# Kernel optimization log

Measured on AMD Instinct MI355X. Metric: run time of the kernel, lower is better.

## Reference

```python
import jax, jax.numpy as jnp
import numpy as np

WH, WW = 7, 7
L = WH * WW            # 49 tokens per window
C = 128                # embedding dim
H = 32                 # heads
HD = C // H            # head dim = 4
BN = 4096              # batch * num_windows


def _relative_position_index(wh, ww):
    coords = np.stack(np.meshgrid(np.arange(wh), np.arange(ww), indexing='ij'))  # [2,wh,ww]
    flat = coords.reshape(2, -1)                     # [2, L]
    rel = flat[:, :, None] - flat[:, None, :]        # [2, L, L]
    rel = rel.transpose(1, 2, 0).copy()              # [L, L, 2]
    rel[:, :, 0] += wh - 1
    rel[:, :, 1] += ww - 1
    rel[:, :, 0] *= 2 * ww - 1
    return jnp.asarray(rel.sum(-1), dtype=jnp.int32)  # [L, L]


REL_IDX = _relative_position_index(WH, WW)


def setup_inputs() -> dict:
    key = jax.random.key(0)
    k1, k2, k3, k4 = jax.random.split(key, 4)
    x = jax.random.normal(k1, (BN, L, C), dtype=jnp.float32)
    W_qkv = jax.random.normal(k2, (C, 3 * C), dtype=jnp.float32) * (C ** -0.5)
    b_qkv = jnp.zeros((3 * C,), dtype=jnp.float32)
    W_proj = jax.random.normal(k3, (C, C), dtype=jnp.float32) * (C ** -0.5)
    b_proj = jnp.zeros((C,), dtype=jnp.float32)
    bias_table = jax.random.normal(k4, ((2 * WH - 1) * (2 * WW - 1), H), dtype=jnp.float32) * 0.02
    return {"x": x, "W_qkv": W_qkv, "b_qkv": b_qkv, "W_proj": W_proj,
            "b_proj": b_proj, "bias_table": bias_table}


def reference(x, W_qkv, b_qkv, W_proj, b_proj, bias_table):
    bn, l, c = x.shape
    scale = HD ** -0.5
    qkv = x @ W_qkv + b_qkv                                   # [BN, L, 3C]
    qkv = qkv.reshape(bn, l, 3, H, HD).transpose(2, 0, 3, 1, 4)  # [3, BN, H, L, HD]
    q, k, v = qkv[0], qkv[1], qkv[2]
    attn = jnp.einsum('bhqd,bhkd->bhqk', q * scale, k)        # [BN, H, L, L]
    rel_bias = bias_table[REL_IDX]                            # [L, L, H]
    attn = attn + rel_bias.transpose(2, 0, 1)[None]           # add [1, H, L, L]
    attn = jax.nn.softmax(attn, axis=-1)
    out = jnp.einsum('bhqk,bhkd->bhqd', attn, v)              # [BN, H, L, HD]
    out = out.transpose(0, 2, 1, 3).reshape(bn, l, c)         # [BN, L, C]
    return out @ W_proj + b_proj
```

## Files before the change

kernel.cpp:

```cpp
#include <hip/hip_runtime.h>
#include <hip/hip_bf16.h>
#include <stdint.h>

#define L 49
#define C 128
#define H 32

typedef __attribute__((ext_vector_type(8))) short bf16x8;
typedef __attribute__((ext_vector_type(4))) float f32x4;

#define XP 136
#define VTP 72
#define QKP 264

#define LOG2E 1.44269504f

__device__ __forceinline__ uint32_t rbits(float f) {
  return __builtin_bit_cast(uint32_t, f) + 0x8000u;
}
__device__ __forceinline__ uint32_t pack2(float a, float b) {
  return __builtin_amdgcn_perm(rbits(b), rbits(a), 0x07060302u);
}
__device__ __forceinline__ ushort bf1(float a) { return (ushort)(rbits(a) >> 16); }

__device__ __forceinline__ bf16x8 mk_frag(uint2 d, bool valid) {
  union { uint32_t u[4]; bf16x8 v; } r;
  r.u[0] = valid ? d.x : 0u;
  r.u[1] = valid ? d.y : 0u;
  r.u[2] = 0u; r.u[3] = 0u;
  return r.v;
}
__device__ __forceinline__ bf16x8 zero8() {
  union { uint32_t u[4]; bf16x8 v; } r;
  r.u[0] = r.u[1] = r.u[2] = r.u[3] = 0u;
  return r.v;
}
__device__ __forceinline__ bf16x8 ones8() {
  union { uint32_t u[4]; bf16x8 v; } r;
  r.u[0] = r.u[1] = r.u[2] = r.u[3] = 0x3F803F80u;
  return r.v;
}

__global__ void __launch_bounds__(256) prep_weights_kernel(
    const float* __restrict__ Wqkv, const float* __restrict__ Wproj,
    ushort* __restrict__ ws) {
  int i = blockIdx.x * 256 + threadIdx.x;
  if (i < 384 * 128) {
    int n = i >> 7, k = i & 127;
    ws[i] = bf1(Wqkv[k * 384 + n]);
  } else {
    int j = i - 384 * 128;
    if (j < 128 * 128) {
      int n = j >> 7, k = j & 127;
      ws[49152 + j] = bf1(Wproj[k * 128 + n]);
    }
  }
}

__global__ void __launch_bounds__(256) prep_bias_kernel(
    const float* __restrict__ bt, float* __restrict__ biasx) {
  int i = blockIdx.x * 256 + threadIdx.x;
  int r = i & 3, lane = (i >> 2) & 63, t = i >> 8;
  int nt = t & 3, mt = (t >> 2) & 3, h = t >> 4;
  int q = nt * 16 + (lane & 15);
  int k = mt * 16 + ((lane >> 4) & 3) * 4 + r;
  float v = -1e30f;
  if (q < L && k < L) {
    int qi = q / 7, qj = q % 7, ki = k / 7, kj = k % 7;
    int idx = (qi - ki + 6) * 13 + (qj - kj + 6);
    v = bt[idx * H + h] * LOG2E;
  }
  biasx[i] = v;
}

__device__ __forceinline__ void head_body(
    f32x4 (&acc)[4][4], int h, const ushort* qk, const ushort* vt,
    char* pw, ushort* qk_mut, int lr, int lg) {
  bf16x8 ka[4], qb[4];
  #pragma unroll
  for (int mt = 0; mt < 4; ++mt) {
    int row = mt * 16 + lr; if (row > 48) row = 48;
    uint2 d = *(const uint2*)&qk[row * QKP + 128 + h * 4];
    ka[mt] = mk_frag(d, lg == 0);
  }
  #pragma unroll
  for (int nt = 0; nt < 4; ++nt) {
    int row = nt * 16 + lr; if (row > 48) row = 48;
    uint2 d = *(const uint2*)&qk[row * QKP + h * 4];
    qb[nt] = mk_frag(d, lg == 0);
  }
  __builtin_amdgcn_s_setprio(1);
  #pragma unroll
  for (int nt = 0; nt < 4; ++nt)
    #pragma unroll
    for (int mt = 0; mt < 4; ++mt)
      acc[mt][nt] = __builtin_amdgcn_mfma_f32_16x16x32_bf16(ka[mt], qb[nt], acc[mt][nt], 0, 0, 0);
  __builtin_amdgcn_s_setprio(0);
  bf16x8 va[2];
  #pragma unroll
  for (int ks = 0; ks < 2; ++ks) {
    bf16x8 t = *(const bf16x8*)&vt[(h * 4 + (lr & 3)) * VTP + ks * 32 + lg * 8];
    va[ks] = (lr < 4) ? t : ((lr == 4) ? ones8() : zero8());
  }
  #pragma unroll
  for (int nt = 0; nt < 4; ++nt) {
    #pragma unroll
    for (int mt = 0; mt < 4; ++mt) {
      uint32_t d0, d1;
      if (mt < 3) {
        uint32_t u0 = rbits(__builtin_amdgcn_exp2f(acc[mt][nt][0]));
        uint32_t u1 = rbits(__builtin_amdgcn_exp2f(acc[mt][nt][1]));
        uint32_t u2 = rbits(__builtin_amdgcn_exp2f(acc[mt][nt][2]));
        uint32_t u3 = rbits(__builtin_amdgcn_exp2f(acc[mt][nt][3]));
        d0 = __builtin_amdgcn_perm(u1, u0, 0x07060302u);
        d1 = __builtin_amdgcn_perm(u3, u2, 0x07060302u);
      } else {
        float e0 = __builtin_amdgcn_exp2f(acc[mt][nt][0]);
        d0 = pack2(e0, 0.0f);
        d1 = 0u;
      }
      int byte = lr * 128 + mt * 32 + lg * 8;
      byte ^= (lr & 7) << 4;
      *(uint2*)(pw + byte) = make_uint2(d0, d1);
    }
    f32x4 oo = {0.f, 0.f, 0.f, 0.f};
    __builtin_amdgcn_s_setprio(1);
    #pragma unroll
    for (int ks = 0; ks < 2; ++ks) {
      int byte = lr * 128 + ks * 64 + lg * 16;
      byte ^= (lr & 7) << 4;
      bf16x8 pb = *(const bf16x8*)(pw + byte);
      oo = __builtin_amdgcn_mfma_f32_16x16x32_bf16(va[ks], pb, oo, 0, 0, 0);
    }
    __builtin_amdgcn_s_setprio(0);
    float den = __shfl_xor(oo[0], 16);
    if (lg == 0) {
      float iv = __builtin_amdgcn_rcpf(den);
      int q = nt * 16 + lr;
      if (q < L) {
        uint2 od = make_uint2(pack2(oo[0] * iv, oo[1] * iv),
                              pack2(oo[2] * iv, oo[3] * iv));
        *(uint2*)&qk_mut[q * QKP + h * 4] = od;
      }
    }
  }
}

__global__ void __launch_bounds__(256, 3) win_attn_kernel(
    const float* __restrict__ x,
    const float* __restrict__ b_qkv,
    const float* __restrict__ b_proj,
    const ushort* __restrict__ wqkvT,
    const ushort* __restrict__ wprojT,
    const float* __restrict__ biasx,
    float* __restrict__ out) {
  __shared__ alignas(16) ushort s_xv[C * VTP];
  __shared__ alignas(16) ushort qk[L * QKP];
  __shared__ alignas(16) ushort p_lds[4][16 * 64];

  ushort* xa = s_xv;
  ushort* vt = s_xv;

  const int tid = threadIdx.x;
  const int w = blockIdx.x;
  const int wv = tid >> 6;
  const int l = tid & 63;
  const int lr = l & 15;
  const int lg = l >> 4;

  {
    const float4* xv = (const float4*)(x + (size_t)w * (L * C));
    for (int i = tid; i < L * C / 4; i += 256) {
      float4 v = xv[i];
      int e = i * 4;
      int r = e >> 7, c = e & 127;
      uint2 u = make_uint2(pack2(v.x, v.y), pack2(v.z, v.w));
      *(uint2*)&xa[r * XP + c] = u;
    }
  }
  __syncthreads();

  {
    bf16x8 af[4][4];
    #pragma unroll
    for (int mt = 0; mt < 4; ++mt) {
      int row = mt * 16 + lr; if (row > 48) row = 48;
      #pragma unroll
      for (int kk = 0; kk < 4; ++kk)
        af[mt][kk] = *(const bf16x8*)&xa[row * XP + kk * 32 + lg * 8];
    }
    __syncthreads();
    #pragma unroll 2
    for (int ntl = 0; ntl < 6; ++ntl) {
      int nt = (ntl < 2) ? (wv * 2 + ntl)
             : (ntl < 4) ? (8 + wv * 2 + (ntl - 2))
                         : (16 + wv * 2 + (ntl - 4));
      int ncol = nt * 16 + lr;
      const ushort* bp = wqkvT + ncol * C + lg * 8;
      bf16x8 b0 = *(const bf16x8*)(bp);
      bf16x8 b1 = *(const bf16x8*)(bp + 32);
      bf16x8 b2 = *(const bf16x8*)(bp + 64);
      bf16x8 b3 = *(const bf16x8*)(bp + 96);
      float bias = b_qkv[ncol];
      float sc = (ncol < 128) ? 0.5f * LOG2E : 1.0f;
      #pragma unroll
      for (int mt = 0; mt < 4; ++mt) {
        f32x4 acc = {0.f, 0.f, 0.f, 0.f};
        acc = __builtin_amdgcn_mfma_f32_16x16x32_bf16(af[mt][0], b0, acc, 0, 0, 0);
        acc = __builtin_amdgcn_mfma_f32_16x16x32_bf16(af[mt][1], b1, acc, 0, 0, 0);
        acc = __builtin_amdgcn_mfma_f32_16x16x32_bf16(af[mt][2], b2, acc, 0, 0, 0);
        acc = __builtin_amdgcn_mfma_f32_16x16x32_bf16(af[mt][3], b3, acc, 0, 0, 0);
        if (ncol < 256) {
          #pragma unroll
          for (int r = 0; r < 4; ++r) {
            int row = mt * 16 + lg * 4 + r;
            if (row < L) qk[row * QKP + ncol] = bf1((acc[r] + bias) * sc);
          }
        } else {
          int kbase = mt * 16 + lg * 4;
          uint2 pv = make_uint2(pack2(acc[0] + bias, acc[1] + bias),
                                pack2(acc[2] + bias, acc[3] + bias));
          *(uint2*)&vt[(ncol - 256) * VTP + kbase] = pv;
        }
      }
    }
  }

  {
    char* pw = (char*)&p_lds[wv][0];
    const f32x4* bx = (const f32x4*)biasx;
    #pragma unroll 2
    for (int hh = 0; hh < 8; ++hh) {
      int h = wv * 8 + hh;
      f32x4 acc[4][4];
      #pragma unroll
      for (int mt = 0; mt < 4; ++mt)
        #pragma unroll
        for (int nt = 0; nt < 4; ++nt)
          acc[mt][nt] = bx[(h * 16 + mt * 4 + nt) * 64 + l];
      head_body(acc, h, qk, vt, pw, qk, lr, lg);
    }
  }
  __syncthreads();

  {
    bf16x8 pf[4][4];
    #pragma unroll
    for (int mt = 0; mt < 4; ++mt) {
      int row = mt * 16 + lr; if (row > 48) row = 48;
      #pragma unroll
      for (int kk = 0; kk < 4; ++kk)
        pf[mt][kk] = *(const bf16x8*)&qk[row * QKP + kk * 32 + lg * 8];
    }
    float* outw = out + (size_t)w * (L * C);
    #pragma unroll 2
    for (int ntl = 0; ntl < 2; ++ntl) {
      int ncol = (wv * 2 + ntl) * 16 + lr;
      const ushort* bp = wprojT + ncol * C + lg * 8;
      bf16x8 b0 = *(const bf16x8*)(bp);
      bf16x8 b1 = *(const bf16x8*)(bp + 32);
      bf16x8 b2 = *(const bf16x8*)(bp + 64);
      bf16x8 b3 = *(const bf16x8*)(bp + 96);
      float bias = b_proj[ncol];
      #pragma unroll
      for (int mt = 0; mt < 4; ++mt) {
        f32x4 acc = {0.f, 0.f, 0.f, 0.f};
        acc = __builtin_amdgcn_mfma_f32_16x16x32_bf16(pf[mt][0], b0, acc, 0, 0, 0);
        acc = __builtin_amdgcn_mfma_f32_16x16x32_bf16(pf[mt][1], b1, acc, 0, 0, 0);
        acc = __builtin_amdgcn_mfma_f32_16x16x32_bf16(pf[mt][2], b2, acc, 0, 0, 0);
        acc = __builtin_amdgcn_mfma_f32_16x16x32_bf16(pf[mt][3], b3, acc, 0, 0, 0);
        #pragma unroll
        for (int r = 0; r < 4; ++r) {
          int row = mt * 16 + lg * 4 + r;
          if (row < L) outw[row * C + ncol] = acc[r] + bias;
        }
      }
    }
  }
}

extern "C" void kernel_launch(void* const* d_in, const int* in_sizes, int n_in,
                              void* d_out, int out_size, void* d_ws, size_t ws_size,
                              hipStream_t stream) {
  const float* x     = (const float*)d_in[0];
  const float* Wqkv  = (const float*)d_in[1];
  const float* bqkv  = (const float*)d_in[2];
  const float* Wproj = (const float*)d_in[3];
  const float* bproj = (const float*)d_in[4];
  const float* btab  = (const float*)d_in[5];
  float* out = (float*)d_out;
  ushort* ws = (ushort*)d_ws;
  float* biasx = (float*)(ws + 65536);

  int bn = in_sizes[0] / (L * C);

  hipLaunchKernelGGL(prep_weights_kernel, dim3(256), dim3(256), 0, stream,
                     Wqkv, Wproj, ws);
  hipLaunchKernelGGL(prep_bias_kernel, dim3(512), dim3(256), 0, stream,
                     btab, biasx);
  hipLaunchKernelGGL(win_attn_kernel, dim3(bn), dim3(256), 0, stream,
                     x, bqkv, bproj, ws, ws + 49152, biasx, out);
}
```

Measured before the change: 170.0 us.

## Make window attention kernel persistent with register prefetch of next window

Turns the one-block-per-window launch into a persistent grid of up to 768 blocks, each looping over windows with stride npers. Within each iteration, the next window's x tile is loaded into registers while the current window's QKV, attention and projection run. This overlaps global loads with compute and removes per-block launch and prologue costs. In exchange it holds 7 float4 values live in registers across the whole loop, which adds register pressure under the 3-blocks-per-CU launch bound and could cause spills or lower occupancy.

```diff
diff --git a/kernel.cpp b/kernel.cpp
--- a/kernel.cpp
+++ b/kernel.cpp
@@ -5,6 +5,7 @@
 #define L 49
 #define C 128
 #define H 32
+#define NPERS 768
 
 typedef __attribute__((ext_vector_type(8))) short bf16x8;
 typedef __attribute__((ext_vector_type(4))) float f32x4;
@@ -153,7 +154,8 @@
     const ushort* __restrict__ wqkvT,
     const ushort* __restrict__ wprojT,
     const float* __restrict__ biasx,
-    float* __restrict__ out) {
+    float* __restrict__ out,
+    int bn, int npers) {
   __shared__ alignas(16) ushort s_xv[C * VTP];
   __shared__ alignas(16) ushort qk[L * QKP];
   __shared__ alignas(16) ushort p_lds[4][16 * 64];
@@ -162,120 +164,142 @@
   ushort* vt = s_xv;
 
   const int tid = threadIdx.x;
-  const int w = blockIdx.x;
   const int wv = tid >> 6;
   const int l = tid & 63;
   const int lr = l & 15;
   const int lg = l >> 4;
 
+  float4 xr[7];
+  int w = blockIdx.x;
   {
     const float4* xv = (const float4*)(x + (size_t)w * (L * C));
-    for (int i = tid; i < L * C / 4; i += 256) {
-      float4 v = xv[i];
-      int e = i * 4;
-      int r = e >> 7, c = e & 127;
-      uint2 u = make_uint2(pack2(v.x, v.y), pack2(v.z, v.w));
-      *(uint2*)&xa[r * XP + c] = u;
-    }
-  }
-  __syncthreads();
-
-  {
-    bf16x8 af[4][4];
-    #pragma unroll
-    for (int mt = 0; mt < 4; ++mt) {
-      int row = mt * 16 + lr; if (row > 48) row = 48;
+    #pragma unroll
+    for (int j = 0; j < 7; ++j) {
+      int i = tid + j * 256;
+      if (i < L * C / 4) xr[j] = xv[i];
+    }
+  }
+
+  for (; w < bn; ) {
+    #pragma unroll
+    for (int j = 0; j < 7; ++j) {
+      int i = tid + j * 256;
+      if (i < L * C / 4) {
+        float4 v = xr[j];
+        int e = i * 4;
+        int r = e >> 7, c = e & 127;
+        *(uint2*)&xa[r * XP + c] = make_uint2(pack2(v.x, v.y), pack2(v.z, v.w));
+      }
+    }
+    const int wn = w + npers;
+    if (wn < bn) {
+      const float4* xv = (const float4*)(x + (size_t)wn * (L * C));
       #pragma unroll
-      for (int kk = 0; kk < 4; ++kk)
-        af[mt][kk] = *(const bf16x8*)&xa[row * XP + kk * 32 + lg * 8];
+      for (int j = 0; j < 7; ++j) {
+        int i = tid + j * 256;
+        if (i < L * C / 4) xr[j] = xv[i];
+      }
     }
     __syncthreads();
-    #pragma unroll 2
-    for (int ntl = 0; ntl < 6; ++ntl) {
-      int nt = (ntl < 2) ? (wv * 2 + ntl)
-             : (ntl < 4) ? (8 + wv * 2 + (ntl - 2))
-                         : (16 + wv * 2 + (ntl - 4));
-      int ncol = nt * 16 + lr;
-      const ushort* bp = wqkvT + ncol * C + lg * 8;
-      bf16x8 b0 = *(const bf16x8*)(bp);
-      bf16x8 b1 = *(const bf16x8*)(bp + 32);
-      bf16x8 b2 = *(const bf16x8*)(bp + 64);
-      bf16x8 b3 = *(const bf16x8*)(bp + 96);
-      float bias = b_qkv[ncol];
-      float sc = (ncol < 128) ? 0.5f * LOG2E : 1.0f;
+
+    {
+      bf16x8 af[4][4];
       #pragma unroll
       for (int mt = 0; mt < 4; ++mt) {
-        f32x4 acc = {0.f, 0.f, 0.f, 0.f};
-        acc = __builtin_amdgcn_mfma_f32_16x16x32_bf16(af[mt][0], b0, acc, 0, 0, 0);
-        acc = __builtin_amdgcn_mfma_f32_16x16x32_bf16(af[mt][1], b1, acc, 0, 0, 0);
-        acc = __builtin_amdgcn_mfma_f32_16x16x32_bf16(af[mt][2], b2, acc, 0, 0, 0);
-        acc = __builtin_amdgcn_mfma_f32_16x16x32_bf16(af[mt][3], b3, acc, 0, 0, 0);
-        if (ncol < 256) {
+        int row = mt * 16 + lr; if (row > 48) row = 48;
+        #pragma unroll
+        for (int kk = 0; kk < 4; ++kk)
+          af[mt][kk] = *(const bf16x8*)&xa[row * XP + kk * 32 + lg * 8];
+      }
+      __syncthreads();
+      #pragma unroll 2
+      for (int ntl = 0; ntl < 6; ++ntl) {
+        int nt = (ntl < 2) ? (wv * 2 + ntl)
+               : (ntl < 4) ? (8 + wv * 2 + (ntl - 2))
+                           : (16 + wv * 2 + (ntl - 4));
+        int ncol = nt * 16 + lr;
+        const ushort* bp = wqkvT + ncol * C + lg * 8;
+        bf16x8 b0 = *(const bf16x8*)(bp);
+        bf16x8 b1 = *(const bf16x8*)(bp + 32);
+        bf16x8 b2 = *(const bf16x8*)(bp + 64);
+        bf16x8 b3 = *(const bf16x8*)(bp + 96);
+        float bias = b_qkv[ncol];
+        float sc = (ncol < 128) ? 0.5f * LOG2E : 1.0f;
+        #pragma unroll
+        for (int mt = 0; mt < 4; ++mt) {
+          f32x4 acc = {0.f, 0.f, 0.f, 0.f};
+          acc = __builtin_amdgcn_mfma_f32_16x16x32_bf16(af[mt][0], b0, acc, 0, 0, 0);
+          acc = __builtin_amdgcn_mfma_f32_16x16x32_bf16(af[mt][1], b1, acc, 0, 0, 0);
+          acc = __builtin_amdgcn_mfma_f32_16x16x32_bf16(af[mt][2], b2, acc, 0, 0, 0);
+          acc = __builtin_amdgcn_mfma_f32_16x16x32_bf16(af[mt][3], b3, acc, 0, 0, 0);
+          if (ncol < 256) {
+            #pragma unroll
+            for (int r = 0; r < 4; ++r) {
+              int row = mt * 16 + lg * 4 + r;
+              if (row < L) qk[row * QKP + ncol] = bf1((acc[r] + bias) * sc);
+            }
+          } else {
+            int kbase = mt * 16 + lg * 4;
+            uint2 pv = make_uint2(pack2(acc[0] + bias, acc[1] + bias),
+                                  pack2(acc[2] + bias, acc[3] + bias));
+            *(uint2*)&vt[(ncol - 256) * VTP + kbase] = pv;
+          }
+        }
+      }
+    }
+
+    {
+      char* pw = (char*)&p_lds[wv][0];
+      const f32x4* bx = (const f32x4*)biasx;
+      #pragma unroll 2
+      for (int hh = 0; hh < 8; ++hh) {
+        int h = wv * 8 + hh;
+        f32x4 acc[4][4];
+        #pragma unroll
+        for (int mt = 0; mt < 4; ++mt)
+          #pragma unroll
+          for (int nt = 0; nt < 4; ++nt)
+            acc[mt][nt] = bx[(h * 16 + mt * 4 + nt) * 64 + l];
+        head_body(acc, h, qk, vt, pw, qk, lr, lg);
+      }
+    }
+    __syncthreads();
+
+    {
+      bf16x8 pf[4][4];
+      #pragma unroll
+      for (int mt = 0; mt < 4; ++mt) {
+        int row = mt * 16 + lr; if (row > 48) row = 48;
+        #pragma unroll
+        for (int kk = 0; kk < 4; ++kk)
+          pf[mt][kk] = *(const bf16x8*)&qk[row * QKP + kk * 32 + lg * 8];
+      }
+      float* outw = out + (size_t)w * (L * C);
+      #pragma unroll 2
+      for (int ntl = 0; ntl < 2; ++ntl) {
+        int ncol = (wv * 2 + ntl) * 16 + lr;
+        const ushort* bp = wprojT + ncol * C + lg * 8;
+        bf16x8 b0 = *(const bf16x8*)(bp);
+        bf16x8 b1 = *(const bf16x8*)(bp + 32);
+        bf16x8 b2 = *(const bf16x8*)(bp + 64);
+        bf16x8 b3 = *(const bf16x8*)(bp + 96);
+        float bias = b_proj[ncol];
+        #pragma unroll
+        for (int mt = 0; mt < 4; ++mt) {
+          f32x4 acc = {0.f, 0.f, 0.f, 0.f};
+          acc = __builtin_amdgcn_mfma_f32_16x16x32_bf16(pf[mt][0], b0, acc, 0, 0, 0);
+          acc = __builtin_amdgcn_mfma_f32_16x16x32_bf16(pf[mt][1], b1, acc, 0, 0, 0);
+          acc = __builtin_amdgcn_mfma_f32_16x16x32_bf16(pf[mt][2], b2, acc, 0, 0, 0);
+          acc = __builtin_amdgcn_mfma_f32_16x16x32_bf16(pf[mt][3], b3, acc, 0, 0, 0);
           #pragma unroll
           for (int r = 0; r < 4; ++r) {
             int row = mt * 16 + lg * 4 + r;
-            if (row < L) qk[row * QKP + ncol] = bf1((acc[r] + bias) * sc);
+            if (row < L) outw[row * C + ncol] = acc[r] + bias;
           }
-        } else {
-          int kbase = mt * 16 + lg * 4;
-          uint2 pv = make_uint2(pack2(acc[0] + bias, acc[1] + bias),
-                                pack2(acc[2] + bias, acc[3] + bias));
-          *(uint2*)&vt[(ncol - 256) * VTP + kbase] = pv;
         }
       }
     }
-  }
-
-  {
-    char* pw = (char*)&p_lds[wv][0];
-    const f32x4* bx = (const f32x4*)biasx;
-    #pragma unroll 2
-    for (int hh = 0; hh < 8; ++hh) {
-      int h = wv * 8 + hh;
-      f32x4 acc[4][4];
-      #pragma unroll
-      for (int mt = 0; mt < 4; ++mt)
-        #pragma unroll
-        for (int nt = 0; nt < 4; ++nt)
-          acc[mt][nt] = bx[(h * 16 + mt * 4 + nt) * 64 + l];
-      head_body(acc, h, qk, vt, pw, qk, lr, lg);
-    }
-  }
-  __syncthreads();
-
-  {
-    bf16x8 pf[4][4];
-    #pragma unroll
-    for (int mt = 0; mt < 4; ++mt) {
-      int row = mt * 16 + lr; if (row > 48) row = 48;
-      #pragma unroll
-      for (int kk = 0; kk < 4; ++kk)
-        pf[mt][kk] = *(const bf16x8*)&qk[row * QKP + kk * 32 + lg * 8];
-    }
-    float* outw = out + (size_t)w * (L * C);
-    #pragma unroll 2
-    for (int ntl = 0; ntl < 2; ++ntl) {
-      int ncol = (wv * 2 + ntl) * 16 + lr;
-      const ushort* bp = wprojT + ncol * C + lg * 8;
-      bf16x8 b0 = *(const bf16x8*)(bp);
-      bf16x8 b1 = *(const bf16x8*)(bp + 32);
-      bf16x8 b2 = *(const bf16x8*)(bp + 64);
-      bf16x8 b3 = *(const bf16x8*)(bp + 96);
-      float bias = b_proj[ncol];
-      #pragma unroll
-      for (int mt = 0; mt < 4; ++mt) {
-        f32x4 acc = {0.f, 0.f, 0.f, 0.f};
-        acc = __builtin_amdgcn_mfma_f32_16x16x32_bf16(pf[mt][0], b0, acc, 0, 0, 0);
-        acc = __builtin_amdgcn_mfma_f32_16x16x32_bf16(pf[mt][1], b1, acc, 0, 0, 0);
-        acc = __builtin_amdgcn_mfma_f32_16x16x32_bf16(pf[mt][2], b2, acc, 0, 0, 0);
-        acc = __builtin_amdgcn_mfma_f32_16x16x32_bf16(pf[mt][3], b3, acc, 0, 0, 0);
-        #pragma unroll
-        for (int r = 0; r < 4; ++r) {
-          int row = mt * 16 + lg * 4 + r;
-          if (row < L) outw[row * C + ncol] = acc[r] + bias;
-        }
-      }
-    }
+    w = wn;
   }
 }
 
@@ -293,11 +317,12 @@
   float* biasx = (float*)(ws + 65536);
 
   int bn = in_sizes[0] / (L * C);
+  int npers = (bn < NPERS) ? bn : NPERS;
 
   hipLaunchKernelGGL(prep_weights_kernel, dim3(256), dim3(256), 0, stream,
                      Wqkv, Wproj, ws);
   hipLaunchKernelGGL(prep_bias_kernel, dim3(512), dim3(256), 0, stream,
                      btab, biasx);
-  hipLaunchKernelGGL(win_attn_kernel, dim3(bn), dim3(256), 0, stream,
-                     x, bqkv, bproj, ws, ws + 49152, biasx, out);
-}
+  hipLaunchKernelGGL(win_attn_kernel, dim3(npers), dim3(256), 0, stream,
+                     x, bqkv, bproj, ws, ws + 49152, biasx, out, bn, npers);
+}
```

After: 301.7 us. +77.4%, slower.
